# Optimization experiments

Measured on AMD Instinct MI355X. Metric: run time of the kernel, lower is better.

## Reference

```python
import jax, jax.numpy as jnp
import numpy as np

B, T, D, H = 2, 2048, 1024, 16
HD = D // H            # head dim = 64
WINDOW = 512           # sliding-window size
EPS = 1e-6
ROPE_BASE = 10000.0


def setup_inputs() -> dict:
    key = jax.random.key(0)
    ks = jax.random.split(key, 5)
    s = 0.02  # init scale for dense kernels
    return {
        "x": jax.random.normal(ks[0], (B, T, D), jnp.float32),
        "Wq": jax.random.normal(ks[1], (D, D), jnp.float32) * s,
        "Wk": jax.random.normal(ks[2], (D, D), jnp.float32) * s,
        "Wv": jax.random.normal(ks[3], (D, D), jnp.float32) * s,
        "Wo": jax.random.normal(ks[4], (D, D), jnp.float32) * s,
        "q_scale": jnp.ones((HD,), jnp.float32),
        "k_scale": jnp.ones((HD,), jnp.float32),
        "sink_logit": jnp.zeros((H,), jnp.float32),
    }


def _rmsnorm(x, scale):
    # x: [..., HD]
    var = jnp.mean(jnp.square(x), axis=-1, keepdims=True)
    return x * jax.lax.rsqrt(var + EPS) * scale


def _rope(x):
    # x: [B, H, T, HD]; standard rotate-half RoPE over the full head dim
    half = HD // 2
    inv_freq = 1.0 / (ROPE_BASE ** (jnp.arange(0, HD, 2, dtype=jnp.float32) / HD))  # [half]
    t = jnp.arange(T, dtype=jnp.float32)
    freqs = t[:, None] * inv_freq[None, :]                # [T, half]
    emb = jnp.concatenate([freqs, freqs], axis=-1)        # [T, HD]
    cos = jnp.cos(emb)[None, None]                        # [1,1,T,HD]
    sin = jnp.sin(emb)[None, None]
    x1, x2 = x[..., :half], x[..., half:]
    rot = jnp.concatenate([-x2, x1], axis=-1)
    return x * cos + rot * sin


def reference(x, Wq, Wk, Wv, Wo, q_scale, k_scale, sink_logit):
    # projections -> [B, T, H, HD]
    q = (x @ Wq).reshape(B, T, H, HD)
    k = (x @ Wk).reshape(B, T, H, HD)
    v = (x @ Wv).reshape(B, T, H, HD)
    # QK RMSNorm over head dim
    q = _rmsnorm(q, q_scale)
    k = _rmsnorm(k, k_scale)
    # -> [B, H, T, HD], then RoPE
    q = _rope(q.transpose(0, 2, 1, 3))
    k = _rope(k.transpose(0, 2, 1, 3))
    v = v.transpose(0, 2, 1, 3)
    # causal sliding-window mask
    idx = jnp.arange(T)
    rel = idx[None, :] - idx[:, None]                     # key - query
    mask = ((rel <= 0) & (rel > -WINDOW))[None, None]     # [1,1,T,T]
    scale = HD ** (-0.5)
    scores = jnp.einsum('bhtd,bhsd->bhts', q, k) * scale
    scores = jnp.where(mask, scores, -jnp.inf)
    # sink-augmented softmax: append per-head sink logit to denominator
    sink = jnp.broadcast_to(sink_logit.reshape(1, H, 1, 1), (B, H, T, 1))
    aug = jnp.concatenate([scores.astype(jnp.float32), sink.astype(jnp.float32)], axis=-1)
    weights = jax.nn.softmax(aug, axis=-1)[..., :T].astype(scores.dtype)
    out = jnp.einsum('bhts,bhsd->bhtd', weights, v)
    out = out.transpose(0, 2, 1, 3).reshape(B, T, D)
    return out @ Wo
```

## Files before the change

kernel.cpp:

```cpp
#include <hip/hip_runtime.h>
#include <math.h>

#define CB 2
#define CT 2048
#define CD 1024
#define CH 16
#define CHD 64
#define CWINDOW 512

typedef __bf16 bf16x8 __attribute__((ext_vector_type(8)));
typedef float floatx4 __attribute__((ext_vector_type(4)));

__device__ __forceinline__ unsigned short f2bf(float f) {
  union { float f; unsigned int u; } v;
  v.f = f;
  unsigned int u = v.u;
  u += 0x7fffu + ((u >> 16) & 1u);
  return (unsigned short)(u >> 16);
}
__device__ __forceinline__ unsigned short f2bf_trunc(float f) {
  union { float f; unsigned int u; } v;
  v.f = f;
  return (unsigned short)(v.u >> 16);
}
__device__ __forceinline__ float bf2f(unsigned int h) {
  union { unsigned int u; float f; } v;
  v.u = h << 16;
  return v.f;
}

__global__ __launch_bounds__(256) void cvt_all(const float* __restrict__ x,
                                               const float* __restrict__ Wq,
                                               const float* __restrict__ Wk,
                                               const float* __restrict__ Wv,
                                               const float* __restrict__ Wo,
                                               unsigned short* __restrict__ xb,
                                               unsigned short* __restrict__ WqT,
                                               unsigned short* __restrict__ WkT,
                                               unsigned short* __restrict__ WvT,
                                               unsigned short* __restrict__ WoT) {
  const int z = blockIdx.z;
  if (z < 4) {
    const float* W = z == 0 ? Wq : z == 1 ? Wk : z == 2 ? Wv : Wo;
    unsigned short* Wt = z == 0 ? WqT : z == 1 ? WkT : z == 2 ? WvT : WoT;
    __shared__ float tile[64][65];
    const int k0 = blockIdx.x * 64, n0 = blockIdx.y * 64;
    const int c = threadIdx.x & 63, r4 = threadIdx.x >> 6;
#pragma unroll
    for (int i = 0; i < 16; ++i) {
      int r = i * 4 + r4;
      tile[r][c] = W[(size_t)(k0 + r) * CD + n0 + c];
    }
    __syncthreads();
#pragma unroll
    for (int i = 0; i < 16; ++i) {
      int r = i * 4 + r4;
      Wt[(size_t)(n0 + r) * CD + k0 + c] = f2bf(tile[c][r]);
    }
  } else {
    const int idx = (z - 4) * 256 + blockIdx.y * 16 + blockIdx.x;
    const int i = idx * 256 + threadIdx.x;
    float4 a = ((const float4*)x)[i * 2];
    float4 b = ((const float4*)x)[i * 2 + 1];
    uint4 o;
    o.x = (unsigned int)f2bf(a.x) | ((unsigned int)f2bf(a.y) << 16);
    o.y = (unsigned int)f2bf(a.z) | ((unsigned int)f2bf(a.w) << 16);
    o.z = (unsigned int)f2bf(b.x) | ((unsigned int)f2bf(b.y) << 16);
    o.w = (unsigned int)f2bf(b.z) | ((unsigned int)f2bf(b.w) << 16);
    ((uint4*)xb)[i] = o;
  }
}

__device__ __forceinline__ void async16(const unsigned short* g, unsigned short* l) {
  __builtin_amdgcn_global_load_lds(
      (const __attribute__((address_space(1))) unsigned int*)g,
      (__attribute__((address_space(3))) unsigned int*)l, 16, 0, 0);
}

template <int MODE, int BM>
__device__ __forceinline__ void mfma_gemm_body(const unsigned short* __restrict__ A,
                                               const unsigned short* __restrict__ Bt,
                                               void* __restrict__ Cout,
                                               const float* __restrict__ scale,
                                               float oscale) {
  constexpr int K = CD;
  constexpr int MT = BM / 32;
  __shared__ unsigned short As[BM * 32];
  __shared__ unsigned short Bs[128 * 32];
  const int tid = threadIdx.x;
  const int wave = tid >> 6, lane = tid & 63;
  const int m0 = blockIdx.x * BM, n0 = blockIdx.y * 128;
  const int mq = (wave & 1) * (BM / 2), nq = (wave >> 1) * 64;

  floatx4 acc[MT][4] = {};
  const int srow = lane >> 2;
  const int skc = (lane & 3) * 8;
  const int fr = lane & 15;
  const int fk = (lane >> 4) * 8;

  for (int k0 = 0; k0 < K; k0 += 32) {
    __syncthreads();
#pragma unroll
    for (int it = 0; it < BM / 64; ++it) {
      const int sub = wave * (BM / 64) + it;
      const int row = sub * 16 + srow;
      async16(A + (size_t)(m0 + row) * K + k0 + skc, &As[sub * 512]);
    }
#pragma unroll
    for (int it = 0; it < 2; ++it) {
      const int sub = wave * 2 + it;
      const int row = sub * 16 + srow;
      async16(Bt + (size_t)(n0 + row) * K + k0 + skc, &Bs[sub * 512]);
    }
    __syncthreads();
    bf16x8 af[MT], bg[4];
#pragma unroll
    for (int mt = 0; mt < MT; ++mt)
      af[mt] = *(const bf16x8*)&As[(mq + mt * 16 + fr) * 32 + fk];
#pragma unroll
    for (int nt = 0; nt < 4; ++nt)
      bg[nt] = *(const bf16x8*)&Bs[(nq + nt * 16 + fr) * 32 + fk];
#pragma unroll
    for (int mt = 0; mt < MT; ++mt)
#pragma unroll
      for (int nt = 0; nt < 4; ++nt)
        acc[mt][nt] = __builtin_amdgcn_mfma_f32_16x16x32_bf16(af[mt], bg[nt], acc[mt][nt], 0, 0, 0);
  }

  if (MODE == 1) {
    const int c = lane & 15;
    const int g = lane >> 4;
    const int hh = (n0 + nq) >> 6;
    const float kf = -0.2878231366242557f;
    const float inv0 = __expf((float)c * kf);
    const float inv1 = __expf((float)(16 + c) * kf);
    float sc[4];
#pragma unroll
    for (int nt = 0; nt < 4; ++nt) sc[nt] = scale[nt * 16 + c];
#pragma unroll
    for (int mt = 0; mt < MT; ++mt) {
#pragma unroll
      for (int i = 0; i < 4; ++i) {
        const int m = m0 + mq + mt * 16 + g * 4 + i;
        const int b = m >> 11, t = m & (CT - 1);
        float v0 = acc[mt][0][i], v1 = acc[mt][1][i];
        float v2 = acc[mt][2][i], v3 = acc[mt][3][i];
        float ss = v0 * v0 + v1 * v1 + v2 * v2 + v3 * v3;
#pragma unroll
        for (int off = 8; off > 0; off >>= 1) ss += __shfl_xor(ss, off);
        const float rs = rsqrtf(ss * (1.0f / 64.0f) + 1e-6f);
        v0 *= rs * sc[0];
        v1 *= rs * sc[1];
        v2 *= rs * sc[2];
        v3 *= rs * sc[3];
        const float tf = (float)t;
        const float a0 = tf * inv0, a1 = tf * inv1;
        const float s0 = __sinf(a0), c0 = __cosf(a0);
        const float s1 = __sinf(a1), c1 = __cosf(a1);
        unsigned short* dst = (unsigned short*)Cout + ((size_t)(b * CH + hh) * CT + t) * CHD;
        ushort4 o;
        o.x = f2bf((v0 * c0 - v2 * s0) * oscale);
        o.y = f2bf((v1 * c1 - v3 * s1) * oscale);
        o.z = f2bf((v2 * c0 + v0 * s0) * oscale);
        o.w = f2bf((v3 * c1 + v1 * s1) * oscale);
        *(ushort4*)&dst[4 * c] = o;
      }
    }
  } else {
#pragma unroll
    for (int mt = 0; mt < MT; ++mt) {
#pragma unroll
      for (int nt = 0; nt < 4; ++nt) {
        const int col = n0 + nq + nt * 16 + (lane & 15);
        if (MODE == 2) {
          const int mb = m0 + mq + mt * 16 + (lane >> 4) * 4;
          const int b = mb >> 11, t = mb & (CT - 1);
          const int h = col >> 6, d = col & 63;
          ushort4 o;
          o.x = f2bf(acc[mt][nt][0]);
          o.y = f2bf(acc[mt][nt][1]);
          o.z = f2bf(acc[mt][nt][2]);
          o.w = f2bf(acc[mt][nt][3]);
          *(ushort4*)&((unsigned short*)Cout)[((size_t)(b * CH + h) * CHD + d) * CT + t] = o;
        } else {
#pragma unroll
          for (int i = 0; i < 4; ++i) {
            const int m = m0 + mq + mt * 16 + (lane >> 4) * 4 + i;
            ((float*)Cout)[(size_t)m * CD + col] = acc[mt][nt][i];
          }
        }
      }
    }
  }
}

__global__ __launch_bounds__(256, 3) void gemm_qkv_mfma(const unsigned short* __restrict__ xb,
                                                        const unsigned short* __restrict__ WqT,
                                                        const unsigned short* __restrict__ WkT,
                                                        const unsigned short* __restrict__ WvT,
                                                        unsigned short* __restrict__ Qh,
                                                        unsigned short* __restrict__ Kh,
                                                        unsigned short* __restrict__ Vt,
                                                        const float* __restrict__ q_scale,
                                                        const float* __restrict__ k_scale) {
  if (blockIdx.z == 2) {
    mfma_gemm_body<2, 128>(xb, WvT, Vt, nullptr, 1.0f);
  } else if (blockIdx.z == 0) {
    mfma_gemm_body<1, 128>(xb, WqT, Qh, q_scale, 0.125f);
  } else {
    mfma_gemm_body<1, 128>(xb, WkT, Kh, k_scale, 1.0f);
  }
}

__global__ __launch_bounds__(256, 3) void gemm_out_mfma(const unsigned short* __restrict__ AO,
                                                        const unsigned short* __restrict__ WoT,
                                                        float* __restrict__ out) {
  mfma_gemm_body<0, 64>(AO, WoT, out, nullptr, 1.0f);
}

__device__ __forceinline__ bf16x8 frag64(const unsigned short* base, int row, int ks, int lane) {
  const int phys = (((ks << 2) + (lane >> 4)) ^ (lane & 7)) << 3;
  return *(const bf16x8*)&base[(row << 6) + phys];
}

__global__ __launch_bounds__(256, 3) void attn_mfma(const unsigned short* __restrict__ Qh,
                                                    const unsigned short* __restrict__ Kh,
                                                    const unsigned short* __restrict__ Vt,
                                                    const float* __restrict__ sink_logit,
                                                    unsigned short* __restrict__ AO) {
  __shared__ unsigned short Qs[128 * 64];
  __shared__ unsigned short Ks[64 * 64];
  __shared__ unsigned short Vs[64 * 64];
  __shared__ unsigned short Ps[128 * 72];

  const int tid = threadIdx.x;
  const int w = tid >> 6, lane = tid & 63;
  const int qb = blockIdx.x, bh = blockIdx.y;
  const int b = bh >> 4, h = bh & 15;
  const int q0 = qb * 128;
  const unsigned short* Qb = Qh + (size_t)bh * CT * CHD;
  const unsigned short* Kb = Kh + (size_t)bh * CT * CHD;
  const unsigned short* Vb = Vt + (size_t)bh * CHD * CT;

  const int l7 = lane & 7, l8 = lane >> 3;
  const int sx8 = (l7 ^ l8) * 8;

#pragma unroll
  for (int s = 0; s < 4; ++s) {
    const int slab = w * 4 + s;
    async16(Qb + (size_t)(q0 + slab * 8 + l8) * CHD + sx8, &Qs[slab * 512]);
  }
  __syncthreads();
  bf16x8 qf[2][2];
#pragma unroll
  for (int nt = 0; nt < 2; ++nt)
#pragma unroll
    for (int ks = 0; ks < 2; ++ks)
      qf[nt][ks] = frag64(Qs, w * 32 + nt * 16 + (lane & 15), ks, lane);

  floatx4 acc[4][2] = {};
  float lsum[2] = {0.f, 0.f};
  const int qw = q0 + w * 32;

  const int kb_lo = (qb >= 4) ? (qb * 2 - 8) : 0;
  const int kb_hi = qb * 2 + 1;
  for (int kb = kb_lo; kb <= kb_hi; ++kb) {
    __syncthreads();
#pragma unroll
    for (int s = 0; s < 2; ++s) {
      const int slab = w * 2 + s;
      const int row = slab * 8 + l8;
      async16(Kb + (size_t)(kb * 64 + row) * CHD + sx8, &Ks[slab * 512]);
      async16(Vb + (size_t)row * CT + kb * 64 + sx8, &Vs[slab * 512]);
    }
    __syncthreads();

    const int kmin = kb * 64, kmax = kb * 64 + 63;
    if (kmin > qw + 31 || kmax <= qw - CWINDOW) continue;

    floatx4 st[4][2] = {};
#pragma unroll
    for (int ks = 0; ks < 2; ++ks) {
      bf16x8 kf[4];
#pragma unroll
      for (int mt = 0; mt < 4; ++mt)
        kf[mt] = frag64(Ks, mt * 16 + (lane & 15), ks, lane);
#pragma unroll
      for (int mt = 0; mt < 4; ++mt)
#pragma unroll
        for (int nt = 0; nt < 2; ++nt)
          st[mt][nt] = __builtin_amdgcn_mfma_f32_16x16x32_bf16(kf[mt], qf[nt][ks], st[mt][nt], 0, 0, 0);
    }

    const bool need_c = (kmax > qw);
    const bool need_w = (kmin <= qw + 31 - CWINDOW);
#pragma unroll
    for (int mt = 0; mt < 4; ++mt) {
#pragma unroll
      for (int nt = 0; nt < 2; ++nt) {
        const int s_base = kb * 64 + mt * 16 + (lane >> 4) * 4;
        const int t_g = q0 + w * 32 + nt * 16 + (lane & 15);
        ushort4 pk;
        float psum = 0.f;
#pragma unroll
        for (int i = 0; i < 4; ++i) {
          float sv = st[mt][nt][i];
          if (need_c || need_w) {
            const int s_g = s_base + i;
            const bool ok = (!need_c || (s_g <= t_g)) && (!need_w || (s_g > t_g - CWINDOW));
            sv = ok ? sv : -INFINITY;
          }
          const unsigned short pb = f2bf_trunc(__expf(sv));
          ((unsigned short*)&pk)[i] = pb;
          psum += bf2f(pb);
        }
        lsum[nt] += psum;
        const int qrow = w * 32 + nt * 16 + (lane & 15);
        const int scol = mt * 16 + (lane >> 4) * 4;
        *(ushort4*)&Ps[qrow * 72 + scol] = pk;
      }
    }

#pragma unroll
    for (int ks = 0; ks < 2; ++ks) {
      bf16x8 vf[4], pf[2];
#pragma unroll
      for (int mt = 0; mt < 4; ++mt)
        vf[mt] = frag64(Vs, mt * 16 + (lane & 15), ks, lane);
#pragma unroll
      for (int nt = 0; nt < 2; ++nt) {
        const int qrow = w * 32 + nt * 16 + (lane & 15);
        pf[nt] = *(const bf16x8*)&Ps[qrow * 72 + ks * 32 + (lane >> 4) * 8];
      }
#pragma unroll
      for (int mt = 0; mt < 4; ++mt)
#pragma unroll
        for (int nt = 0; nt < 2; ++nt)
          acc[mt][nt] = __builtin_amdgcn_mfma_f32_16x16x32_bf16(vf[mt], pf[nt], acc[mt][nt], 0, 0, 0);
    }
  }

  const float sinkw = __expf(sink_logit[h]);
  float inv[2];
#pragma unroll
  for (int nt = 0; nt < 2; ++nt) {
    float l = lsum[nt];
    l += __shfl_xor(l, 16);
    l += __shfl_xor(l, 32);
    inv[nt] = 1.0f / (l + sinkw);
  }
#pragma unroll
  for (int mt = 0; mt < 4; ++mt) {
#pragma unroll
    for (int nt = 0; nt < 2; ++nt) {
      const int t_g = q0 + w * 32 + nt * 16 + (lane & 15);
      const int d0 = mt * 16 + (lane >> 4) * 4;
      ushort4 o;
      o.x = f2bf(acc[mt][nt][0] * inv[nt]);
      o.y = f2bf(acc[mt][nt][1] * inv[nt]);
      o.z = f2bf(acc[mt][nt][2] * inv[nt]);
      o.w = f2bf(acc[mt][nt][3] * inv[nt]);
      *(ushort4*)&AO[(size_t)(b * CT + t_g) * CD + h * CHD + d0] = o;
    }
  }
}

extern "C" void kernel_launch(void* const* d_in, const int* in_sizes, int n_in,
                              void* d_out, int out_size, void* d_ws, size_t ws_size,
                              hipStream_t stream) {
  (void)in_sizes;
  (void)n_in;
  (void)out_size;
  (void)ws_size;
  const float* x = (const float*)d_in[0];
  const float* Wq = (const float*)d_in[1];
  const float* Wk = (const float*)d_in[2];
  const float* Wv = (const float*)d_in[3];
  const float* Wo = (const float*)d_in[4];
  const float* q_scale = (const float*)d_in[5];
  const float* k_scale = (const float*)d_in[6];
  const float* sink = (const float*)d_in[7];
  float* out = (float*)d_out;

  const size_t per = (size_t)CB * CH * CT * CHD;
  unsigned short* Qh = (unsigned short*)d_ws;
  unsigned short* Kh = Qh + per;
  unsigned short* Vt = Kh + per;
  unsigned short* AO = Vt + per;
  unsigned short* xb = AO + per;
  unsigned short* WqT = xb + per;
  unsigned short* WkT = WqT + (size_t)CD * CD;
  unsigned short* WvT = WkT + (size_t)CD * CD;
  unsigned short* WoT = WvT + (size_t)CD * CD;

  dim3 blk(256);
  cvt_all<<<dim3(16, 16, 12), blk, 0, stream>>>(x, Wq, Wk, Wv, Wo, xb, WqT, WkT, WvT, WoT);
  gemm_qkv_mfma<<<dim3(32, 8, 3), blk, 0, stream>>>(xb, WqT, WkT, WvT, Qh, Kh, Vt, q_scale, k_scale);
  attn_mfma<<<dim3(CT / 128, CB * CH), blk, 0, stream>>>(Qh, Kh, Vt, sink, AO);
  gemm_out_mfma<<<dim3(64, 8), blk, 0, stream>>>(AO, WoT, out);
}
```

Before: 169.7 us.

## Double-buffer K/V tiles in attention and raise MFMA priority

The attention kernel now keeps two K/V tile buffers in shared memory and issues async loads for the next key block before computing on the current one. The two barriers per iteration become a single vmcnt wait plus barrier, so global-load latency can overlap the MFMA work. s_setprio is raised around the MFMA bursts. In exchange, shared memory per block grows and the launch-bounds occupancy hint drops from 3 to 2 blocks per CU, which may reduce latency hiding across waves.

```diff
diff --git a/kernel.cpp b/kernel.cpp
--- a/kernel.cpp
+++ b/kernel.cpp
@@ -223,14 +223,14 @@
   return *(const bf16x8*)&base[(row << 6) + phys];
 }
 
-__global__ __launch_bounds__(256, 3) void attn_mfma(const unsigned short* __restrict__ Qh,
+__global__ __launch_bounds__(256, 2) void attn_mfma(const unsigned short* __restrict__ Qh,
                                                     const unsigned short* __restrict__ Kh,
                                                     const unsigned short* __restrict__ Vt,
                                                     const float* __restrict__ sink_logit,
                                                     unsigned short* __restrict__ AO) {
   __shared__ unsigned short Qs[128 * 64];
-  __shared__ unsigned short Ks[64 * 64];
-  __shared__ unsigned short Vs[64 * 64];
+  __shared__ unsigned short Ks[2][64 * 64];
+  __shared__ unsigned short Vs[2][64 * 64];
   __shared__ unsigned short Ps[128 * 72];
 
   const int tid = threadIdx.x;
@@ -245,12 +245,23 @@
   const int l7 = lane & 7, l8 = lane >> 3;
   const int sx8 = (l7 ^ l8) * 8;
 
+  const int kb_lo = (qb >= 4) ? (qb * 2 - 8) : 0;
+  const int kb_hi = qb * 2 + 1;
+
 #pragma unroll
   for (int s = 0; s < 4; ++s) {
     const int slab = w * 4 + s;
     async16(Qb + (size_t)(q0 + slab * 8 + l8) * CHD + sx8, &Qs[slab * 512]);
   }
+#pragma unroll
+  for (int s = 0; s < 2; ++s) {
+    const int slab = w * 2 + s;
+    const int row = slab * 8 + l8;
+    async16(Kb + (size_t)(kb_lo * 64 + row) * CHD + sx8, &Ks[0][slab * 512]);
+    async16(Vb + (size_t)row * CT + kb_lo * 64 + sx8, &Vs[0][slab * 512]);
+  }
   __syncthreads();
+
   bf16x8 qf[2][2];
 #pragma unroll
   for (int nt = 0; nt < 2; ++nt)
@@ -262,82 +273,92 @@
   float lsum[2] = {0.f, 0.f};
   const int qw = q0 + w * 32;
 
-  const int kb_lo = (qb >= 4) ? (qb * 2 - 8) : 0;
-  const int kb_hi = qb * 2 + 1;
+  int cur = 0;
   for (int kb = kb_lo; kb <= kb_hi; ++kb) {
-    __syncthreads();
-#pragma unroll
-    for (int s = 0; s < 2; ++s) {
-      const int slab = w * 2 + s;
-      const int row = slab * 8 + l8;
-      async16(Kb + (size_t)(kb * 64 + row) * CHD + sx8, &Ks[slab * 512]);
-      async16(Vb + (size_t)row * CT + kb * 64 + sx8, &Vs[slab * 512]);
-    }
-    __syncthreads();
+    if (kb < kb_hi) {
+#pragma unroll
+      for (int s = 0; s < 2; ++s) {
+        const int slab = w * 2 + s;
+        const int row = slab * 8 + l8;
+        async16(Kb + (size_t)((kb + 1) * 64 + row) * CHD + sx8, &Ks[cur ^ 1][slab * 512]);
+        async16(Vb + (size_t)row * CT + (kb + 1) * 64 + sx8, &Vs[cur ^ 1][slab * 512]);
+      }
+    }
 
     const int kmin = kb * 64, kmax = kb * 64 + 63;
-    if (kmin > qw + 31 || kmax <= qw - CWINDOW) continue;
-
-    floatx4 st[4][2] = {};
-#pragma unroll
-    for (int ks = 0; ks < 2; ++ks) {
-      bf16x8 kf[4];
-#pragma unroll
-      for (int mt = 0; mt < 4; ++mt)
-        kf[mt] = frag64(Ks, mt * 16 + (lane & 15), ks, lane);
-#pragma unroll
-      for (int mt = 0; mt < 4; ++mt)
-#pragma unroll
-        for (int nt = 0; nt < 2; ++nt)
-          st[mt][nt] = __builtin_amdgcn_mfma_f32_16x16x32_bf16(kf[mt], qf[nt][ks], st[mt][nt], 0, 0, 0);
-    }
-
-    const bool need_c = (kmax > qw);
-    const bool need_w = (kmin <= qw + 31 - CWINDOW);
-#pragma unroll
-    for (int mt = 0; mt < 4; ++mt) {
-#pragma unroll
-      for (int nt = 0; nt < 2; ++nt) {
-        const int s_base = kb * 64 + mt * 16 + (lane >> 4) * 4;
-        const int t_g = q0 + w * 32 + nt * 16 + (lane & 15);
-        ushort4 pk;
-        float psum = 0.f;
-#pragma unroll
-        for (int i = 0; i < 4; ++i) {
-          float sv = st[mt][nt][i];
-          if (need_c || need_w) {
-            const int s_g = s_base + i;
-            const bool ok = (!need_c || (s_g <= t_g)) && (!need_w || (s_g > t_g - CWINDOW));
-            sv = ok ? sv : -INFINITY;
+    if (!(kmin > qw + 31 || kmax <= qw - CWINDOW)) {
+      const unsigned short* Kc = Ks[cur];
+      const unsigned short* Vc = Vs[cur];
+
+      floatx4 st[4][2] = {};
+#pragma unroll
+      for (int ks = 0; ks < 2; ++ks) {
+        bf16x8 kf[4];
+#pragma unroll
+        for (int mt = 0; mt < 4; ++mt)
+          kf[mt] = frag64(Kc, mt * 16 + (lane & 15), ks, lane);
+        __builtin_amdgcn_s_setprio(1);
+#pragma unroll
+        for (int mt = 0; mt < 4; ++mt)
+#pragma unroll
+          for (int nt = 0; nt < 2; ++nt)
+            st[mt][nt] = __builtin_amdgcn_mfma_f32_16x16x32_bf16(kf[mt], qf[nt][ks], st[mt][nt], 0, 0, 0);
+        __builtin_amdgcn_s_setprio(0);
+      }
+
+      const bool need_c = (kmax > qw);
+      const bool need_w = (kmin <= qw + 31 - CWINDOW);
+#pragma unroll
+      for (int mt = 0; mt < 4; ++mt) {
+#pragma unroll
+        for (int nt = 0; nt < 2; ++nt) {
+          const int s_base = kb * 64 + mt * 16 + (lane >> 4) * 4;
+          const int t_g = q0 + w * 32 + nt * 16 + (lane & 15);
+          ushort4 pk;
+          float psum = 0.f;
+#pragma unroll
+          for (int i = 0; i < 4; ++i) {
+            float sv = st[mt][nt][i];
+            if (need_c || need_w) {
+              const int s_g = s_base + i;
+              const bool ok = (!need_c || (s_g <= t_g)) && (!need_w || (s_g > t_g - CWINDOW));
+              sv = ok ? sv : -INFINITY;
+            }
+            const unsigned short pb = f2bf_trunc(__expf(sv));
+            ((unsigned short*)&pk)[i] = pb;
+            psum += bf2f(pb);
           }
-          const unsigned short pb = f2bf_trunc(__expf(sv));
-          ((unsigned short*)&pk)[i] = pb;
-          psum += bf2f(pb);
+          lsum[nt] += psum;
+          const int qrow = w * 32 + nt * 16 + (lane & 15);
+          const int scol = mt * 16 + (lane >> 4) * 4;
+          *(ushort4*)&Ps[qrow * 72 + scol] = pk;
         }
-        lsum[nt] += psum;
-        const int qrow = w * 32 + nt * 16 + (lane & 15);
-        const int scol = mt * 16 + (lane >> 4) * 4;
-        *(ushort4*)&Ps[qrow * 72 + scol] = pk;
-      }
-    }
-
-#pragma unroll
-    for (int ks = 0; ks < 2; ++ks) {
-      bf16x8 vf[4], pf[2];
-#pragma unroll
-      for (int mt = 0; mt < 4; ++mt)
-        vf[mt] = frag64(Vs, mt * 16 + (lane & 15), ks, lane);
-#pragma unroll
-      for (int nt = 0; nt < 2; ++nt) {
-        const int qrow = w * 32 + nt * 16 + (lane & 15);
-        pf[nt] = *(const bf16x8*)&Ps[qrow * 72 + ks * 32 + (lane >> 4) * 8];
-      }
-#pragma unroll
-      for (int mt = 0; mt < 4; ++mt)
-#pragma unroll
-        for (int nt = 0; nt < 2; ++nt)
-          acc[mt][nt] = __builtin_amdgcn_mfma_f32_16x16x32_bf16(vf[mt], pf[nt], acc[mt][nt], 0, 0, 0);
-    }
+      }
+
+#pragma unroll
+      for (int ks = 0; ks < 2; ++ks) {
+        bf16x8 vf[4], pf[2];
+#pragma unroll
+        for (int mt = 0; mt < 4; ++mt)
+          vf[mt] = frag64(Vc, mt * 16 + (lane & 15), ks, lane);
+#pragma unroll
+        for (int nt = 0; nt < 2; ++nt) {
+          const int qrow = w * 32 + nt * 16 + (lane & 15);
+          pf[nt] = *(const bf16x8*)&Ps[qrow * 72 + ks * 32 + (lane >> 4) * 8];
+        }
+        __builtin_amdgcn_s_setprio(1);
+#pragma unroll
+        for (int mt = 0; mt < 4; ++mt)
+#pragma unroll
+          for (int nt = 0; nt < 2; ++nt)
+            acc[mt][nt] = __builtin_amdgcn_mfma_f32_16x16x32_bf16(vf[mt], pf[nt], acc[mt][nt], 0, 0, 0);
+        __builtin_amdgcn_s_setprio(0);
+      }
+    }
+
+    asm volatile("s_waitcnt vmcnt(0)" ::: "memory");
+    __builtin_amdgcn_s_barrier();
+    cur ^= 1;
   }
 
   const float sinkw = __expf(sink_logit[h]);
```

New measurement: 168.1 us. About the same (-0.9%).
